# Performance work log

Hardware: AMD Instinct MI355X
Metric: run time of the kernel (lower is better)

## Reference

```python
import jax, jax.numpy as jnp
import numpy as np

# pywt db4 decomposition filters (w.dec_lo / w.dec_hi), full precision
DEC_LO = np.array([-0.010597401784997278, 0.032883011666982945, 0.030841381835986965,
                   -0.18703481171888114, -0.02798376941698385, 0.6308807679295904,
                   0.7148465705525415, 0.23037781330885523], dtype=np.float32)
DEC_HI = np.array([-0.23037781330885523, 0.7148465705525415, -0.6308807679295904,
                   -0.02798376941698385, 0.18703481171888114, 0.030841381835986965,
                   -0.032883011666982945, -0.010597401784997278], dtype=np.float32)
FLEN = 8
LEVELS = 4
# kernel for lax correlation == pywt convolution => use reversed dec filters
_KERN = np.stack([DEC_LO[::-1], DEC_HI[::-1]])[:, None, :]  # [2, 1, F]


def _dwt_step(x):
    """Single-level DWT matching pywt.dwt(x, 'db4', mode='symmetric').
    x: [N, L] -> (cA, cD) each [N, (L+F-1)//2].
    pywt: symmetric-extend by F-1 per side, full convolution with dec filter,
    keep conv[F-1:-(F-1)][1::2]  ==  correlation(ext[:,1:], reversed_filter, stride 2).
    """
    ext = jnp.pad(x, ((0, 0), (FLEN - 1, FLEN - 1)), mode='symmetric')[:, 1:]
    out = jax.lax.conv_general_dilated(
        ext[:, None, :],                      # [N, 1, Lext-1]
        jnp.asarray(_KERN, dtype=x.dtype),    # [2, 1, F]
        window_strides=(2,), padding='VALID') # [N, 2, o]
    return out[:, 0, :], out[:, 1, :]


def _features(c):
    """6 statistical features per signal. c: [N, L] -> [N, 6]."""
    absc = jnp.abs(c)
    sq = c * c
    mean_abs = absc.mean(-1)
    std = jnp.std(c, axis=-1)               # population std, matches np.std
    rms = jnp.sqrt(sq.mean(-1))
    mx = absc.max(-1)
    energy = sq.sum(-1)
    zc = (jnp.diff(jnp.sign(c), axis=-1) != 0).sum(-1).astype(c.dtype) / c.shape[-1]
    return jnp.stack([mean_abs, std, rms, mx, energy, zc], axis=-1)


def _wavelet_features(x2d):
    """x2d: [N, T] -> [N, 6*(LEVELS+1)] in pywt.wavedec coeff order."""
    cA = x2d
    cds = []
    for _ in range(LEVELS):
        cA, cD = _dwt_step(cA)
        cds.append(cD)
    coeffs = [cA] + cds[::-1]  # [cA4, cD4, cD3, cD2, cD1]
    return jnp.concatenate([_features(c) for c in coeffs], axis=-1)


def setup_inputs() -> dict:
    key = jax.random.key(0)
    x = jax.random.normal(key, (64, 64, 16384), dtype=jnp.float32)
    return {"x": x}


def reference(x):
    B, C, T = x.shape
    feats = _wavelet_features(x.reshape(B * C, T))  # [B*C, 30]
    return feats.reshape(B, C, -1)                  # [B, C, 30]
```

## Files before the change

kernel.cpp:

```cpp
#include <hip/hip_runtime.h>


#define T0 16384
#define BLK 512
#define NW (BLK / 64)

constexpr float FLO[8] = {
     0.23037781330885523f,  0.7148465705525415f,   0.6308807679295904f,
    -0.02798376941698385f, -0.18703481171888114f,  0.030841381835986965f,
     0.032883011666982945f, -0.010597401784997278f };
constexpr float FHI[8] = {
    -0.010597401784997278f, -0.032883011666982945f, 0.030841381835986965f,
     0.18703481171888114f,  -0.02798376941698385f,  -0.6308807679295904f,
     0.7148465705525415f,   -0.23037781330885523f };

__device__ __forceinline__ float getsym(const float* __restrict__ s, int t, int L) {
    if (t < 0) t = -1 - t;
    else if (t >= L) t = 2 * L - 1 - t;
    return s[t];
}

__device__ __forceinline__ float zcstep(float p, float q) {
    return ((__float_as_int(p) ^ __float_as_int(q)) < 0) ? 1.f : 0.f;
}

__device__ __forceinline__ void band_reduce(float sabs, float ssum, float ssq,
                                            float smax, float zc,
                                            int band, float* __restrict__ red) {
    #pragma unroll
    for (int off = 32; off > 0; off >>= 1) {
        sabs += __shfl_xor(sabs, off, 64);
        ssum += __shfl_xor(ssum, off, 64);
        ssq  += __shfl_xor(ssq,  off, 64);
        smax  = fmaxf(smax, __shfl_xor(smax, off, 64));
        zc   += __shfl_xor(zc,   off, 64);
    }
    const int lane = threadIdx.x & 63;
    const int wave = threadIdx.x >> 6;
    if (lane == 0) {
        float* r = red + (band * NW + wave) * 5;
        r[0] = sabs; r[1] = ssum; r[2] = ssq; r[3] = smax; r[4] = zc;
    }
}

template<bool LAST>
__device__ __forceinline__ void dwt_quad_level(const float* __restrict__ src, int L,
                                               float* __restrict__ dst, int o,
                                               int dband, float* __restrict__ red) {
    float sabs = 0.f, ssum = 0.f, ssq = 0.f, smax = 0.f, zc = 0.f;
    float sabsA = 0.f, ssumA = 0.f, ssqA = 0.f, smaxA = 0.f, zcA = 0.f;
    const int nq_main = (o - 1) >> 2;

    for (int k = threadIdx.x; k < nq_main; k += BLK) {
        const int w = 8 * k - 8;
        float v[20];
        if (w >= 0 && w + 20 <= L) {
            #pragma unroll
            for (int q = 0; q < 5; ++q) {
                const float4 t = *reinterpret_cast<const float4*>(src + w + 4 * q);
                v[4*q+0] = t.x; v[4*q+1] = t.y; v[4*q+2] = t.z; v[4*q+3] = t.w;
            }
        } else {
            #pragma unroll
            for (int j = 2; j < 18; ++j) v[j] = getsym(src, w + j, L);
        }
        float a[5], d[5];
        #pragma unroll
        for (int i = 0; i < 5; ++i) { a[i] = 0.f; d[i] = 0.f; }
        #pragma unroll
        for (int i = 0; i < 4; ++i) {
            #pragma unroll
            for (int m = 0; m < 8; ++m) {
                a[i] = fmaf(v[2*i+2+m], FLO[m], a[i]);
                d[i] = fmaf(v[2*i+2+m], FHI[m], d[i]);
            }
        }
        #pragma unroll
        for (int m = 0; m < 8; ++m) {
            d[4] = fmaf(v[10+m], FHI[m], d[4]);
            if constexpr (LAST) a[4] = fmaf(v[10+m], FLO[m], a[4]);
        }
        if constexpr (!LAST) {
            *reinterpret_cast<float4*>(dst + 4 * k) = make_float4(a[0], a[1], a[2], a[3]);
        }
        #pragma unroll
        for (int i = 0; i < 4; ++i) {
            const float ad = fabsf(d[i]);
            sabs += ad; ssum += d[i]; ssq = fmaf(d[i], d[i], ssq);
            smax = fmaxf(smax, ad);
            zc += zcstep(d[i], d[i+1]);
            if constexpr (LAST) {
                const float aa = fabsf(a[i]);
                sabsA += aa; ssumA += a[i]; ssqA = fmaf(a[i], a[i], ssqA);
                smaxA = fmaxf(smaxA, aa);
                zcA += zcstep(a[i], a[i+1]);
            }
        }
    }

    if (threadIdx.x == BLK - 1) {
        const int k = nq_main;
        const int w = 8 * k - 8;
        float v[20];
        #pragma unroll
        for (int j = 2; j < 18; ++j) v[j] = getsym(src, w + j, L);
        float a[5], d[5];
        #pragma unroll
        for (int i = 0; i < 5; ++i) { a[i] = 0.f; d[i] = 0.f; }
        #pragma unroll
        for (int i = 0; i < 5; ++i) {
            #pragma unroll
            for (int m = 0; m < 8; ++m) {
                a[i] = fmaf(v[2*i+2+m], FLO[m], a[i]);
                d[i] = fmaf(v[2*i+2+m], FHI[m], d[i]);
            }
        }
        #pragma unroll
        for (int i = 0; i < 4; ++i) {
            const int p = 4 * k + i;
            if (p < o) {
                const float ad = fabsf(d[i]);
                sabs += ad; ssum += d[i]; ssq = fmaf(d[i], d[i], ssq);
                smax = fmaxf(smax, ad);
                if (p + 1 < o) zc += zcstep(d[i], d[i+1]);
                if constexpr (LAST) {
                    const float aa = fabsf(a[i]);
                    sabsA += aa; ssumA += a[i]; ssqA = fmaf(a[i], a[i], ssqA);
                    smaxA = fmaxf(smaxA, aa);
                    if (p + 1 < o) zcA += zcstep(a[i], a[i+1]);
                } else {
                    dst[p] = a[i];
                }
            }
        }
    }

    band_reduce(sabs, ssum, ssq, smax, zc, dband, red);
    if constexpr (LAST) band_reduce(sabsA, ssumA, ssqA, smaxA, zcA, 0, red);
}

__global__ void __launch_bounds__(BLK, 6)
wavelet_feat_kernel(const float* __restrict__ x, float* __restrict__ out) {
    __shared__ __align__(16) float A[8196];
    __shared__ __align__(16) float B[4104];
    __shared__ float red[5 * NW * 5];

    const int sig = blockIdx.x;
    const float* src0 = x + (size_t)sig * T0;
    float* outp = out + (size_t)sig * 30;

    dwt_quad_level<false>(src0, T0,   A, 8195, 4, red);
    __syncthreads();
    dwt_quad_level<false>(A,    8195, B, 4101, 3, red);
    __syncthreads();
    dwt_quad_level<false>(B,    4101, A, 2054, 2, red);
    __syncthreads();
    dwt_quad_level<true >(A,    2054, nullptr, 1030, 1, red);
    __syncthreads();

    if (threadIdx.x < 5) {
        const int band = threadIdx.x;
        float a = 0.f, s = 0.f, q = 0.f, m = 0.f, z = 0.f;
        #pragma unroll
        for (int w = 0; w < NW; ++w) {
            const float* r = red + (band * NW + w) * 5;
            a += r[0]; s += r[1]; q += r[2]; m = fmaxf(m, r[3]); z += r[4];
        }
        const int o = (band <= 1) ? 1030 : (band == 2 ? 2054 : (band == 3 ? 4101 : 8195));
        const float inv  = 1.0f / (float)o;
        const float mean = s * inv;
        const float var  = q * inv - mean * mean;
        float* op = outp + band * 6;
        op[0] = a * inv;
        op[1] = sqrtf(fmaxf(var, 0.f));
        op[2] = sqrtf(q * inv);
        op[3] = m;
        op[4] = q;
        op[5] = z * inv;
    }
}

extern "C" void kernel_launch(void* const* d_in, const int* in_sizes, int n_in,
                              void* d_out, int out_size, void* d_ws, size_t ws_size,
                              hipStream_t stream) {
    const float* x = (const float*)d_in[0];
    float* out = (float*)d_out;
    const int nsig = in_sizes[0] / T0;
    hipLaunchKernelGGL(wavelet_feat_kernel, dim3(nsig), dim3(BLK), 0, stream, x, out);
}
```

Baseline: 90.06 us.

## Run DWT levels in place in one LDS buffer and reduce via ds_swizzle

```diff
diff --git a/kernel.cpp b/kernel.cpp
--- a/kernel.cpp
+++ b/kernel.cpp
@@ -3,7 +3,6 @@
 
 #define T0 16384
 #define BLK 512
-#define NW (BLK / 64)
 
 constexpr float FLO[8] = {
      0.23037781330885523f,  0.7148465705525415f,   0.6308807679295904f,
@@ -27,143 +26,196 @@
 __device__ __forceinline__ void band_reduce(float sabs, float ssum, float ssq,
                                             float smax, float zc,
                                             int band, float* __restrict__ red) {
-    #pragma unroll
-    for (int off = 32; off > 0; off >>= 1) {
-        sabs += __shfl_xor(sabs, off, 64);
-        ssum += __shfl_xor(ssum, off, 64);
-        ssq  += __shfl_xor(ssq,  off, 64);
-        smax  = fmaxf(smax, __shfl_xor(smax, off, 64));
-        zc   += __shfl_xor(zc,   off, 64);
-    }
-    const int lane = threadIdx.x & 63;
-    const int wave = threadIdx.x >> 6;
-    if (lane == 0) {
-        float* r = red + (band * NW + wave) * 5;
+#define SWZF(v, PAT) __int_as_float(__builtin_amdgcn_ds_swizzle(__float_as_int(v), PAT))
+#define RSTEP(PAT) \
+    sabs += SWZF(sabs, PAT); \
+    ssum += SWZF(ssum, PAT); \
+    ssq  += SWZF(ssq,  PAT); \
+    smax  = fmaxf(smax, SWZF(smax, PAT)); \
+    zc   += SWZF(zc,   PAT);
+    RSTEP(0x041F) RSTEP(0x081F) RSTEP(0x101F) RSTEP(0x201F) RSTEP(0x401F)
+#undef RSTEP
+#undef SWZF
+    if ((threadIdx.x & 31) == 0) {
+        float* r = red + (band * 16 + ((int)threadIdx.x >> 5)) * 5;
         r[0] = sabs; r[1] = ssum; r[2] = ssq; r[3] = smax; r[4] = zc;
     }
 }
 
+__device__ __forceinline__ void load_win(const float* __restrict__ src, int L, int k,
+                                         float* __restrict__ v) {
+    const int w = 8 * k - 8;
+    if (w >= 0 && w + 20 <= L) {
+        #pragma unroll
+        for (int q = 0; q < 5; ++q) {
+            const float4 t = *reinterpret_cast<const float4*>(src + w + 4 * q);
+            v[4*q+0] = t.x; v[4*q+1] = t.y; v[4*q+2] = t.z; v[4*q+3] = t.w;
+        }
+    } else {
+        #pragma unroll
+        for (int j = 2; j < 18; ++j) v[j] = getsym(src, w + j, L);
+    }
+}
+
 template<bool LAST>
-__device__ __forceinline__ void dwt_quad_level(const float* __restrict__ src, int L,
-                                               float* __restrict__ dst, int o,
-                                               int dband, float* __restrict__ red) {
+__device__ __forceinline__ void quad_dots(const float* __restrict__ v,
+                                          float* __restrict__ a, float* __restrict__ d) {
+    #pragma unroll
+    for (int i = 0; i < 5; ++i) { a[i] = 0.f; d[i] = 0.f; }
+    #pragma unroll
+    for (int i = 0; i < 4; ++i) {
+        #pragma unroll
+        for (int m = 0; m < 8; ++m) {
+            a[i] = fmaf(v[2*i+2+m], FLO[m], a[i]);
+            d[i] = fmaf(v[2*i+2+m], FHI[m], d[i]);
+        }
+    }
+    #pragma unroll
+    for (int m = 0; m < 8; ++m) {
+        d[4] = fmaf(v[10+m], FHI[m], d[4]);
+        if constexpr (LAST) a[4] = fmaf(v[10+m], FLO[m], a[4]);
+    }
+}
+
+__device__ void dwt_l1(const float* __restrict__ x, float* __restrict__ A,
+                       float* __restrict__ red) {
     float sabs = 0.f, ssum = 0.f, ssq = 0.f, smax = 0.f, zc = 0.f;
-    float sabsA = 0.f, ssumA = 0.f, ssqA = 0.f, smaxA = 0.f, zcA = 0.f;
-    const int nq_main = (o - 1) >> 2;
-
-    for (int k = threadIdx.x; k < nq_main; k += BLK) {
-        const int w = 8 * k - 8;
-        float v[20];
-        if (w >= 0 && w + 20 <= L) {
-            #pragma unroll
-            for (int q = 0; q < 5; ++q) {
-                const float4 t = *reinterpret_cast<const float4*>(src + w + 4 * q);
-                v[4*q+0] = t.x; v[4*q+1] = t.y; v[4*q+2] = t.z; v[4*q+3] = t.w;
-            }
-        } else {
-            #pragma unroll
-            for (int j = 2; j < 18; ++j) v[j] = getsym(src, w + j, L);
-        }
-        float a[5], d[5];
-        #pragma unroll
-        for (int i = 0; i < 5; ++i) { a[i] = 0.f; d[i] = 0.f; }
-        #pragma unroll
-        for (int i = 0; i < 4; ++i) {
-            #pragma unroll
-            for (int m = 0; m < 8; ++m) {
-                a[i] = fmaf(v[2*i+2+m], FLO[m], a[i]);
-                d[i] = fmaf(v[2*i+2+m], FHI[m], d[i]);
-            }
-        }
-        #pragma unroll
-        for (int m = 0; m < 8; ++m) {
-            d[4] = fmaf(v[10+m], FHI[m], d[4]);
-            if constexpr (LAST) a[4] = fmaf(v[10+m], FLO[m], a[4]);
-        }
-        if constexpr (!LAST) {
-            *reinterpret_cast<float4*>(dst + 4 * k) = make_float4(a[0], a[1], a[2], a[3]);
-        }
+    const int L = T0;
+    for (int k = (int)threadIdx.x; k < 2048; k += BLK) {
+        float v[20], a[5], d[5];
+        load_win(x, L, k, v);
+        quad_dots<false>(v, a, d);
+        *reinterpret_cast<float4*>(A + 4 * k) = make_float4(a[0], a[1], a[2], a[3]);
         #pragma unroll
         for (int i = 0; i < 4; ++i) {
             const float ad = fabsf(d[i]);
             sabs += ad; ssum += d[i]; ssq = fmaf(d[i], d[i], ssq);
             smax = fmaxf(smax, ad);
-            zc += zcstep(d[i], d[i+1]);
-            if constexpr (LAST) {
-                const float aa = fabsf(a[i]);
-                sabsA += aa; ssumA += a[i]; ssqA = fmaf(a[i], a[i], ssqA);
-                smaxA = fmaxf(smaxA, aa);
-                zcA += zcstep(a[i], a[i+1]);
-            }
-        }
-    }
-
+            zc += zcstep(d[i], d[i + 1]);
+        }
+    }
     if (threadIdx.x == BLK - 1) {
-        const int k = nq_main;
-        const int w = 8 * k - 8;
-        float v[20];
-        #pragma unroll
-        for (int j = 2; j < 18; ++j) v[j] = getsym(src, w + j, L);
-        float a[5], d[5];
-        #pragma unroll
-        for (int i = 0; i < 5; ++i) { a[i] = 0.f; d[i] = 0.f; }
-        #pragma unroll
-        for (int i = 0; i < 5; ++i) {
-            #pragma unroll
-            for (int m = 0; m < 8; ++m) {
-                a[i] = fmaf(v[2*i+2+m], FLO[m], a[i]);
-                d[i] = fmaf(v[2*i+2+m], FHI[m], d[i]);
-            }
-        }
+        const int k = 2048;
+        float v[20], a[5], d[5];
+        #pragma unroll
+        for (int j = 2; j < 18; ++j) v[j] = getsym(x, 8 * k - 8 + j, L);
+        quad_dots<false>(v, a, d);
+        #pragma unroll
+        for (int m = 0; m < 8; ++m) a[4] = fmaf(v[10 + m], FLO[m], a[4]);
         #pragma unroll
         for (int i = 0; i < 4; ++i) {
             const int p = 4 * k + i;
-            if (p < o) {
+            if (p < 8195) {
+                A[p] = a[i];
                 const float ad = fabsf(d[i]);
                 sabs += ad; ssum += d[i]; ssq = fmaf(d[i], d[i], ssq);
                 smax = fmaxf(smax, ad);
-                if (p + 1 < o) zc += zcstep(d[i], d[i+1]);
+                if (p + 1 < 8195) zc += zcstep(d[i], d[i + 1]);
+            }
+        }
+    }
+    band_reduce(sabs, ssum, ssq, smax, zc, 4, red);
+}
+
+template<bool LAST, int L, int o, int DBAND>
+__device__ __forceinline__ void dwt_ip(float* __restrict__ A, float* __restrict__ red) {
+    float sabs = 0.f, ssum = 0.f, ssq = 0.f, smax = 0.f, zc = 0.f;
+    float sabsA = 0.f, ssumA = 0.f, ssqA = 0.f, smaxA = 0.f, zcA = 0.f;
+    constexpr int NQ  = (o - 1) >> 2;
+    constexpr int NCH = (NQ + BLK - 1) / BLK;
+    const int tid = (int)threadIdx.x;
+
+    float ap[4];  int wk = -1;
+    float tq[4];  bool tw = false;
+
+    #pragma unroll
+    for (int c = 0; c < NCH; ++c) {
+        const int k = c * BLK + tid;
+        wk = -1;
+        if (k < NQ) {
+            float v[20], a[5], d[5];
+            load_win(A, L, k, v);
+            quad_dots<LAST>(v, a, d);
+            #pragma unroll
+            for (int i = 0; i < 4; ++i) {
+                const float ad = fabsf(d[i]);
+                sabs += ad; ssum += d[i]; ssq = fmaf(d[i], d[i], ssq);
+                smax = fmaxf(smax, ad);
+                zc += zcstep(d[i], d[i + 1]);
                 if constexpr (LAST) {
                     const float aa = fabsf(a[i]);
                     sabsA += aa; ssumA += a[i]; ssqA = fmaf(a[i], a[i], ssqA);
                     smaxA = fmaxf(smaxA, aa);
-                    if (p + 1 < o) zcA += zcstep(a[i], a[i+1]);
-                } else {
-                    dst[p] = a[i];
+                    zcA += zcstep(a[i], a[i + 1]);
                 }
             }
-        }
-    }
-
-    band_reduce(sabs, ssum, ssq, smax, zc, dband, red);
+            ap[0] = a[0]; ap[1] = a[1]; ap[2] = a[2]; ap[3] = a[3];
+            wk = k;
+        }
+        if (c == NCH - 1 && tid == BLK - 1) {
+            float v[20], a[5], d[5];
+            #pragma unroll
+            for (int j = 2; j < 18; ++j) v[j] = getsym(A, 8 * NQ - 8 + j, L);
+            quad_dots<true>(v, a, d);
+            #pragma unroll
+            for (int i = 0; i < 4; ++i) {
+                const int p = 4 * NQ + i;
+                if (p < o) {
+                    const float ad = fabsf(d[i]);
+                    sabs += ad; ssum += d[i]; ssq = fmaf(d[i], d[i], ssq);
+                    smax = fmaxf(smax, ad);
+                    if (p + 1 < o) zc += zcstep(d[i], d[i + 1]);
+                    if constexpr (LAST) {
+                        const float aa = fabsf(a[i]);
+                        sabsA += aa; ssumA += a[i]; ssqA = fmaf(a[i], a[i], ssqA);
+                        smaxA = fmaxf(smaxA, aa);
+                        if (p + 1 < o) zcA += zcstep(a[i], a[i + 1]);
+                    }
+                }
+                tq[i] = a[i];
+            }
+            tw = true;
+        }
+        if constexpr (!LAST) {
+            __syncthreads();
+            if (wk >= 0)
+                *reinterpret_cast<float4*>(A + 4 * wk) = make_float4(ap[0], ap[1], ap[2], ap[3]);
+            if (tw) {
+                #pragma unroll
+                for (int i = 0; i < 4; ++i)
+                    if (4 * NQ + i < o) A[4 * NQ + i] = tq[i];
+                tw = false;
+            }
+        }
+    }
+    band_reduce(sabs, ssum, ssq, smax, zc, DBAND, red);
     if constexpr (LAST) band_reduce(sabsA, ssumA, ssqA, smaxA, zcA, 0, red);
 }
 
-__global__ void __launch_bounds__(BLK, 6)
+__global__ void __launch_bounds__(BLK, 8)
 wavelet_feat_kernel(const float* __restrict__ x, float* __restrict__ out) {
     __shared__ __align__(16) float A[8196];
-    __shared__ __align__(16) float B[4104];
-    __shared__ float red[5 * NW * 5];
+    __shared__ float red[5 * 16 * 5];
 
     const int sig = blockIdx.x;
     const float* src0 = x + (size_t)sig * T0;
     float* outp = out + (size_t)sig * 30;
 
-    dwt_quad_level<false>(src0, T0,   A, 8195, 4, red);
-    __syncthreads();
-    dwt_quad_level<false>(A,    8195, B, 4101, 3, red);
-    __syncthreads();
-    dwt_quad_level<false>(B,    4101, A, 2054, 2, red);
-    __syncthreads();
-    dwt_quad_level<true >(A,    2054, nullptr, 1030, 1, red);
+    dwt_l1(src0, A, red);
+    __syncthreads();
+    dwt_ip<false, 8195, 4101, 3>(A, red);
+    __syncthreads();
+    dwt_ip<false, 4101, 2054, 2>(A, red);
+    __syncthreads();
+    dwt_ip<true,  2054, 1030, 1>(A, red);
     __syncthreads();
 
     if (threadIdx.x < 5) {
-        const int band = threadIdx.x;
+        const int band = (int)threadIdx.x;
         float a = 0.f, s = 0.f, q = 0.f, m = 0.f, z = 0.f;
         #pragma unroll
-        for (int w = 0; w < NW; ++w) {
-            const float* r = red + (band * NW + w) * 5;
+        for (int h = 0; h < 16; ++h) {
+            const float* r = red + (band * 16 + h) * 5;
             a += r[0]; s += r[1]; q += r[2]; m = fmaxf(m, r[3]); z += r[4];
         }
         const int o = (band <= 1) ? 1030 : (band == 2 ? 2054 : (band == 3 ? 4101 : 8195));
```

Measured after the change: 103.6 us. 1.15x slower.

## Compute DWT levels in place in registers to drop second LDS buffer

Applied to the files above, without the earlier changes.

```diff
diff --git a/kernel.cpp b/kernel.cpp
--- a/kernel.cpp
+++ b/kernel.cpp
@@ -43,6 +43,55 @@
     }
 }
 
+__device__ __forceinline__ void load_win(const float* __restrict__ src, int L, int k,
+                                         float* __restrict__ v) {
+    const int w = 8 * k - 8;
+    if (w >= 0 && w + 20 <= L) {
+        #pragma unroll
+        for (int q = 0; q < 5; ++q) {
+            const float4 t = *reinterpret_cast<const float4*>(src + w + 4 * q);
+            v[4*q+0] = t.x; v[4*q+1] = t.y; v[4*q+2] = t.z; v[4*q+3] = t.w;
+        }
+    } else {
+        #pragma unroll
+        for (int j = 2; j < 18; ++j) v[j] = getsym(src, w + j, L);
+    }
+}
+
+template<bool LAST>
+__device__ __forceinline__ void quad_dots(const float* __restrict__ v,
+                                          float* __restrict__ a, float* __restrict__ d) {
+    #pragma unroll
+    for (int i = 0; i < 5; ++i) { a[i] = 0.f; d[i] = 0.f; }
+    #pragma unroll
+    for (int i = 0; i < 4; ++i) {
+        #pragma unroll
+        for (int m = 0; m < 8; ++m) {
+            a[i] = fmaf(v[2*i+2+m], FLO[m], a[i]);
+            d[i] = fmaf(v[2*i+2+m], FHI[m], d[i]);
+        }
+    }
+    #pragma unroll
+    for (int m = 0; m < 8; ++m) {
+        d[4] = fmaf(v[10+m], FHI[m], d[4]);
+        if constexpr (LAST) a[4] = fmaf(v[10+m], FLO[m], a[4]);
+    }
+}
+
+__device__ __forceinline__ void quad_dots_tail(const float* __restrict__ v,
+                                               float* __restrict__ a, float* __restrict__ d) {
+    #pragma unroll
+    for (int i = 0; i < 5; ++i) { a[i] = 0.f; d[i] = 0.f; }
+    #pragma unroll
+    for (int i = 0; i < 5; ++i) {
+        #pragma unroll
+        for (int m = 0; m < 8; ++m) {
+            a[i] = fmaf(v[2*i+2+m], FLO[m], a[i]);
+            d[i] = fmaf(v[2*i+2+m], FHI[m], d[i]);
+        }
+    }
+}
+
 template<bool LAST>
 __device__ __forceinline__ void dwt_quad_level(const float* __restrict__ src, int L,
                                                float* __restrict__ dst, int o,
@@ -52,34 +101,9 @@
     const int nq_main = (o - 1) >> 2;
 
     for (int k = threadIdx.x; k < nq_main; k += BLK) {
-        const int w = 8 * k - 8;
-        float v[20];
-        if (w >= 0 && w + 20 <= L) {
-            #pragma unroll
-            for (int q = 0; q < 5; ++q) {
-                const float4 t = *reinterpret_cast<const float4*>(src + w + 4 * q);
-                v[4*q+0] = t.x; v[4*q+1] = t.y; v[4*q+2] = t.z; v[4*q+3] = t.w;
-            }
-        } else {
-            #pragma unroll
-            for (int j = 2; j < 18; ++j) v[j] = getsym(src, w + j, L);
-        }
-        float a[5], d[5];
-        #pragma unroll
-        for (int i = 0; i < 5; ++i) { a[i] = 0.f; d[i] = 0.f; }
-        #pragma unroll
-        for (int i = 0; i < 4; ++i) {
-            #pragma unroll
-            for (int m = 0; m < 8; ++m) {
-                a[i] = fmaf(v[2*i+2+m], FLO[m], a[i]);
-                d[i] = fmaf(v[2*i+2+m], FHI[m], d[i]);
-            }
-        }
-        #pragma unroll
-        for (int m = 0; m < 8; ++m) {
-            d[4] = fmaf(v[10+m], FHI[m], d[4]);
-            if constexpr (LAST) a[4] = fmaf(v[10+m], FLO[m], a[4]);
-        }
+        float v[20], a[5], d[5];
+        load_win(src, L, k, v);
+        quad_dots<LAST>(v, a, d);
         if constexpr (!LAST) {
             *reinterpret_cast<float4*>(dst + 4 * k) = make_float4(a[0], a[1], a[2], a[3]);
         }
@@ -88,33 +112,22 @@
             const float ad = fabsf(d[i]);
             sabs += ad; ssum += d[i]; ssq = fmaf(d[i], d[i], ssq);
             smax = fmaxf(smax, ad);
-            zc += zcstep(d[i], d[i+1]);
+            zc += zcstep(d[i], d[i + 1]);
             if constexpr (LAST) {
                 const float aa = fabsf(a[i]);
                 sabsA += aa; ssumA += a[i]; ssqA = fmaf(a[i], a[i], ssqA);
                 smaxA = fmaxf(smaxA, aa);
-                zcA += zcstep(a[i], a[i+1]);
+                zcA += zcstep(a[i], a[i + 1]);
             }
         }
     }
 
     if (threadIdx.x == BLK - 1) {
         const int k = nq_main;
-        const int w = 8 * k - 8;
-        float v[20];
-        #pragma unroll
-        for (int j = 2; j < 18; ++j) v[j] = getsym(src, w + j, L);
-        float a[5], d[5];
-        #pragma unroll
-        for (int i = 0; i < 5; ++i) { a[i] = 0.f; d[i] = 0.f; }
-        #pragma unroll
-        for (int i = 0; i < 5; ++i) {
-            #pragma unroll
-            for (int m = 0; m < 8; ++m) {
-                a[i] = fmaf(v[2*i+2+m], FLO[m], a[i]);
-                d[i] = fmaf(v[2*i+2+m], FHI[m], d[i]);
-            }
-        }
+        float v[20], a[5], d[5];
+        #pragma unroll
+        for (int j = 2; j < 18; ++j) v[j] = getsym(src, 8 * k - 8 + j, L);
+        quad_dots_tail(v, a, d);
         #pragma unroll
         for (int i = 0; i < 4; ++i) {
             const int p = 4 * k + i;
@@ -139,27 +152,88 @@
     if constexpr (LAST) band_reduce(sabsA, ssumA, ssqA, smaxA, zcA, 0, red);
 }
 
-__global__ void __launch_bounds__(BLK, 6)
+template<int L, int o, int DBAND>
+__device__ __forceinline__ void dwt_hold_level(float* __restrict__ A,
+                                               float* __restrict__ red) {
+    float sabs = 0.f, ssum = 0.f, ssq = 0.f, smax = 0.f, zc = 0.f;
+    constexpr int NQ = (o - 1) >> 2;
+    constexpr int NI = (NQ + BLK - 1) / BLK;
+    const int tid = (int)threadIdx.x;
+
+    float hq[NI][4];
+    float tq[4];
+
+    #pragma unroll
+    for (int c = 0; c < NI; ++c) {
+        const int k = c * BLK + tid;
+        if (k < NQ) {
+            float v[20], a[5], d[5];
+            load_win(A, L, k, v);
+            quad_dots<false>(v, a, d);
+            #pragma unroll
+            for (int i = 0; i < 4; ++i) {
+                const float ad = fabsf(d[i]);
+                sabs += ad; ssum += d[i]; ssq = fmaf(d[i], d[i], ssq);
+                smax = fmaxf(smax, ad);
+                zc += zcstep(d[i], d[i + 1]);
+                hq[c][i] = a[i];
+            }
+        }
+    }
+    if (tid == BLK - 1) {
+        float v[20], a[5], d[5];
+        #pragma unroll
+        for (int j = 2; j < 18; ++j) v[j] = getsym(A, 8 * NQ - 8 + j, L);
+        quad_dots_tail(v, a, d);
+        #pragma unroll
+        for (int i = 0; i < 4; ++i) {
+            const int p = 4 * NQ + i;
+            if (p < o) {
+                const float ad = fabsf(d[i]);
+                sabs += ad; ssum += d[i]; ssq = fmaf(d[i], d[i], ssq);
+                smax = fmaxf(smax, ad);
+                if (p + 1 < o) zc += zcstep(d[i], d[i + 1]);
+            }
+            tq[i] = a[i];
+        }
+    }
+
+    __syncthreads();
+    #pragma unroll
+    for (int c = 0; c < NI; ++c) {
+        const int k = c * BLK + tid;
+        if (k < NQ)
+            *reinterpret_cast<float4*>(A + 4 * k) =
+                make_float4(hq[c][0], hq[c][1], hq[c][2], hq[c][3]);
+    }
+    if (tid == BLK - 1) {
+        #pragma unroll
+        for (int i = 0; i < 4; ++i)
+            if (4 * NQ + i < o) A[4 * NQ + i] = tq[i];
+    }
+    __syncthreads();
+
+    band_reduce(sabs, ssum, ssq, smax, zc, DBAND, red);
+}
+
+__global__ void __launch_bounds__(BLK, 8)
 wavelet_feat_kernel(const float* __restrict__ x, float* __restrict__ out) {
     __shared__ __align__(16) float A[8196];
-    __shared__ __align__(16) float B[4104];
     __shared__ float red[5 * NW * 5];
 
     const int sig = blockIdx.x;
     const float* src0 = x + (size_t)sig * T0;
     float* outp = out + (size_t)sig * 30;
 
-    dwt_quad_level<false>(src0, T0,   A, 8195, 4, red);
-    __syncthreads();
-    dwt_quad_level<false>(A,    8195, B, 4101, 3, red);
-    __syncthreads();
-    dwt_quad_level<false>(B,    4101, A, 2054, 2, red);
-    __syncthreads();
-    dwt_quad_level<true >(A,    2054, nullptr, 1030, 1, red);
+    dwt_quad_level<false>(src0, T0, A, 8195, 4, red);
+    __syncthreads();
+    dwt_hold_level<8195, 4101, 3>(A, red);
+    dwt_hold_level<4101, 2054, 2>(A, red);
+    dwt_quad_level<true>(A, 2054, nullptr, 1030, 1, red);
     __syncthreads();
 
     if (threadIdx.x < 5) {
-        const int band = threadIdx.x;
+        const int band = (int)threadIdx.x;
         float a = 0.f, s = 0.f, q = 0.f, m = 0.f, z = 0.f;
         #pragma unroll
         for (int w = 0; w < NW; ++w) {
```

Result: slower. 131.3 us (+45.8%).

## Give each thread a contiguous span per level with swizzled LDS and bitmask zero-crossings

Applied to the files above, without the earlier changes.

```diff
diff --git a/kernel.cpp b/kernel.cpp
--- a/kernel.cpp
+++ b/kernel.cpp
@@ -14,152 +14,167 @@
      0.18703481171888114f,  -0.02798376941698385f,  -0.6308807679295904f,
      0.7148465705525415f,   -0.23037781330885523f };
 
-__device__ __forceinline__ float getsym(const float* __restrict__ s, int t, int L) {
-    if (t < 0) t = -1 - t;
-    else if (t >= L) t = 2 * L - 1 - t;
-    return s[t];
-}
-
-__device__ __forceinline__ float zcstep(float p, float q) {
-    return ((__float_as_int(p) ^ __float_as_int(q)) < 0) ? 1.f : 0.f;
-}
-
-__device__ __forceinline__ void band_reduce(float sabs, float ssum, float ssq,
-                                            float smax, float zc,
-                                            int band, float* __restrict__ red) {
+#define SWZ(i4) ((i4) ^ (((i4) >> 3) & 7))
+
+__device__ __forceinline__ float4 lds_read4(const float* __restrict__ A, int i4) {
+    return reinterpret_cast<const float4*>(A)[SWZ(i4)];
+}
+__device__ __forceinline__ void lds_write4(float* __restrict__ A, int i4, float4 t) {
+    reinterpret_cast<float4*>(A)[SWZ(i4)] = t;
+}
+__device__ __forceinline__ void lds_write1(float* __restrict__ A, int f, float t) {
+    A[4 * SWZ(f >> 2) + (f & 3)] = t;
+}
+
+struct Acc { float sabs, ssum, ssq, smax, zc; };
+
+__device__ __forceinline__ void band_reduce(Acc a, int band, float* __restrict__ red) {
     #pragma unroll
     for (int off = 32; off > 0; off >>= 1) {
-        sabs += __shfl_xor(sabs, off, 64);
-        ssum += __shfl_xor(ssum, off, 64);
-        ssq  += __shfl_xor(ssq,  off, 64);
-        smax  = fmaxf(smax, __shfl_xor(smax, off, 64));
-        zc   += __shfl_xor(zc,   off, 64);
+        a.sabs += __shfl_xor(a.sabs, off, 64);
+        a.ssum += __shfl_xor(a.ssum, off, 64);
+        a.ssq  += __shfl_xor(a.ssq,  off, 64);
+        a.smax  = fmaxf(a.smax, __shfl_xor(a.smax, off, 64));
+        a.zc   += __shfl_xor(a.zc,   off, 64);
     }
     const int lane = threadIdx.x & 63;
     const int wave = threadIdx.x >> 6;
     if (lane == 0) {
         float* r = red + (band * NW + wave) * 5;
-        r[0] = sabs; r[1] = ssum; r[2] = ssq; r[3] = smax; r[4] = zc;
-    }
-}
-
-template<bool LAST>
-__device__ __forceinline__ void dwt_quad_level(const float* __restrict__ src, int L,
-                                               float* __restrict__ dst, int o,
-                                               int dband, float* __restrict__ red) {
-    float sabs = 0.f, ssum = 0.f, ssq = 0.f, smax = 0.f, zc = 0.f;
-    float sabsA = 0.f, ssumA = 0.f, ssqA = 0.f, smaxA = 0.f, zcA = 0.f;
-    const int nq_main = (o - 1) >> 2;
-
-    for (int k = threadIdx.x; k < nq_main; k += BLK) {
-        const int w = 8 * k - 8;
-        float v[20];
-        if (w >= 0 && w + 20 <= L) {
-            #pragma unroll
-            for (int q = 0; q < 5; ++q) {
-                const float4 t = *reinterpret_cast<const float4*>(src + w + 4 * q);
-                v[4*q+0] = t.x; v[4*q+1] = t.y; v[4*q+2] = t.z; v[4*q+3] = t.w;
+        r[0] = a.sabs; r[1] = a.ssum; r[2] = a.ssq; r[3] = a.smax; r[4] = a.zc;
+    }
+}
+
+template<int NOUT, bool EXTRA, bool LAST, bool VECW>
+__device__ __forceinline__ void span_core(const float* __restrict__ v,
+                                          float* __restrict__ dst, int p0,
+                                          Acc& aD, Acc& aA) {
+    unsigned dm = 0, am = 0;
+    float aq[4];
+    #pragma unroll
+    for (int i = 0; i < NOUT; ++i) {
+        float a = 0.f, d = 0.f;
+        #pragma unroll
+        for (int m = 0; m < 8; ++m) {
+            a = fmaf(v[2*i+2+m], FLO[m], a);
+            d = fmaf(v[2*i+2+m], FHI[m], d);
+        }
+        dm = (dm << 1) | (__float_as_uint(d) >> 31);
+        aD.sabs += fabsf(d); aD.ssum += d; aD.ssq = fmaf(d, d, aD.ssq);
+        aD.smax = fmaxf(aD.smax, fabsf(d));
+        if constexpr (LAST) {
+            am = (am << 1) | (__float_as_uint(a) >> 31);
+            aA.sabs += fabsf(a); aA.ssum += a; aA.ssq = fmaf(a, a, aA.ssq);
+            aA.smax = fmaxf(aA.smax, fabsf(a));
+        } else if constexpr (VECW) {
+            aq[i & 3] = a;
+            if ((i & 3) == 3)
+                lds_write4(dst, (p0 >> 2) + (i >> 2),
+                           make_float4(aq[0], aq[1], aq[2], aq[3]));
+        } else {
+            lds_write1(dst, p0 + i, a);
+        }
+    }
+    if constexpr (EXTRA) {
+        float d = 0.f;
+        #pragma unroll
+        for (int m = 0; m < 8; ++m) d = fmaf(v[2*NOUT+2+m], FHI[m], d);
+        dm = (dm << 1) | (__float_as_uint(d) >> 31);
+        if constexpr (LAST) {
+            float a = 0.f;
+            #pragma unroll
+            for (int m = 0; m < 8; ++m) a = fmaf(v[2*NOUT+2+m], FLO[m], a);
+            am = (am << 1) | (__float_as_uint(a) >> 31);
+        }
+    }
+    constexpr int NP = EXTRA ? NOUT : NOUT - 1;
+    if constexpr (NP > 0) {
+        aD.zc += (float)__popc((dm ^ (dm >> 1)) & ((1u << NP) - 1u));
+        if constexpr (LAST)
+            aA.zc += (float)__popc((am ^ (am >> 1)) & ((1u << NP) - 1u));
+    }
+}
+
+template<int S, int NT, int L, int o, bool LAST, bool GSRC>
+__device__ __forceinline__ void dwt_level(const float* __restrict__ src,
+                                          float* __restrict__ dst,
+                                          int dband, float* __restrict__ red) {
+    Acc aD = {0.f, 0.f, 0.f, 0.f, 0.f};
+    Acc aA = {0.f, 0.f, 0.f, 0.f, 0.f};
+    const int t = (int)threadIdx.x;
+    constexpr int SN = o - S * (NT - 1);
+
+    if (t < NT - 1) {
+        constexpr int NF = S / 2 + 3;
+        float v[4 * NF];
+        const int w = 2 * S * t - 8;
+        if (t == 0) {
+            #pragma unroll
+            for (int q = 0; q < NF - 2; ++q) {
+                float4 f;
+                if constexpr (GSRC) f = *reinterpret_cast<const float4*>(src + 4 * q);
+                else                f = lds_read4(src, q);
+                v[8+4*q] = f.x; v[9+4*q] = f.y; v[10+4*q] = f.z; v[11+4*q] = f.w;
             }
+            #pragma unroll
+            for (int j = 0; j < 8; ++j) v[j] = v[15 - j];
         } else {
             #pragma unroll
-            for (int j = 2; j < 18; ++j) v[j] = getsym(src, w + j, L);
-        }
-        float a[5], d[5];
-        #pragma unroll
-        for (int i = 0; i < 5; ++i) { a[i] = 0.f; d[i] = 0.f; }
-        #pragma unroll
-        for (int i = 0; i < 4; ++i) {
-            #pragma unroll
-            for (int m = 0; m < 8; ++m) {
-                a[i] = fmaf(v[2*i+2+m], FLO[m], a[i]);
-                d[i] = fmaf(v[2*i+2+m], FHI[m], d[i]);
+            for (int q = 0; q < NF; ++q) {
+                float4 f;
+                if constexpr (GSRC) f = *reinterpret_cast<const float4*>(src + w + 4 * q);
+                else                f = lds_read4(src, (w >> 2) + q);
+                v[4*q] = f.x; v[4*q+1] = f.y; v[4*q+2] = f.z; v[4*q+3] = f.w;
             }
         }
-        #pragma unroll
-        for (int m = 0; m < 8; ++m) {
-            d[4] = fmaf(v[10+m], FHI[m], d[4]);
-            if constexpr (LAST) a[4] = fmaf(v[10+m], FLO[m], a[4]);
-        }
-        if constexpr (!LAST) {
-            *reinterpret_cast<float4*>(dst + 4 * k) = make_float4(a[0], a[1], a[2], a[3]);
-        }
-        #pragma unroll
-        for (int i = 0; i < 4; ++i) {
-            const float ad = fabsf(d[i]);
-            sabs += ad; ssum += d[i]; ssq = fmaf(d[i], d[i], ssq);
-            smax = fmaxf(smax, ad);
-            zc += zcstep(d[i], d[i+1]);
-            if constexpr (LAST) {
-                const float aa = fabsf(a[i]);
-                sabsA += aa; ssumA += a[i]; ssqA = fmaf(a[i], a[i], ssqA);
-                smaxA = fmaxf(smaxA, aa);
-                zcA += zcstep(a[i], a[i+1]);
+        span_core<S, true, LAST, true>(v, dst, S * t, aD, aA);
+    } else if (t == NT - 1) {
+        constexpr int NFt = (2 * SN + 8 + 3) / 4;
+        constexpr int p0 = S * (NT - 1);
+        constexpr int w  = 2 * p0 - 8;
+        constexpr int JM = L - w;
+        float v[4 * NFt];
+        #pragma unroll
+        for (int q = 0; q < NFt; ++q) {
+            if (!GSRC || (w + 4 * q + 4 <= L)) {
+                float4 f;
+                if constexpr (GSRC) f = *reinterpret_cast<const float4*>(src + w + 4 * q);
+                else                f = lds_read4(src, (w >> 2) + q);
+                v[4*q] = f.x; v[4*q+1] = f.y; v[4*q+2] = f.z; v[4*q+3] = f.w;
             }
         }
-    }
-
-    if (threadIdx.x == BLK - 1) {
-        const int k = nq_main;
-        const int w = 8 * k - 8;
-        float v[20];
-        #pragma unroll
-        for (int j = 2; j < 18; ++j) v[j] = getsym(src, w + j, L);
-        float a[5], d[5];
-        #pragma unroll
-        for (int i = 0; i < 5; ++i) { a[i] = 0.f; d[i] = 0.f; }
-        #pragma unroll
-        for (int i = 0; i < 5; ++i) {
-            #pragma unroll
-            for (int m = 0; m < 8; ++m) {
-                a[i] = fmaf(v[2*i+2+m], FLO[m], a[i]);
-                d[i] = fmaf(v[2*i+2+m], FHI[m], d[i]);
-            }
-        }
-        #pragma unroll
-        for (int i = 0; i < 4; ++i) {
-            const int p = 4 * k + i;
-            if (p < o) {
-                const float ad = fabsf(d[i]);
-                sabs += ad; ssum += d[i]; ssq = fmaf(d[i], d[i], ssq);
-                smax = fmaxf(smax, ad);
-                if (p + 1 < o) zc += zcstep(d[i], d[i+1]);
-                if constexpr (LAST) {
-                    const float aa = fabsf(a[i]);
-                    sabsA += aa; ssumA += a[i]; ssqA = fmaf(a[i], a[i], ssqA);
-                    smaxA = fmaxf(smaxA, aa);
-                    if (p + 1 < o) zcA += zcstep(a[i], a[i+1]);
-                } else {
-                    dst[p] = a[i];
-                }
-            }
-        }
-    }
-
-    band_reduce(sabs, ssum, ssq, smax, zc, dband, red);
-    if constexpr (LAST) band_reduce(sabsA, ssumA, ssqA, smaxA, zcA, 0, red);
+        #pragma unroll
+        for (int j = JM; j < 4 * NFt; ++j)
+            v[j] = v[2 * JM - 1 - j];
+        span_core<SN, false, LAST, false>(v, dst, p0, aD, aA);
+    }
+
+    band_reduce(aD, dband, red);
+    if constexpr (LAST) band_reduce(aA, 0, red);
 }
 
 __global__ void __launch_bounds__(BLK, 6)
 wavelet_feat_kernel(const float* __restrict__ x, float* __restrict__ out) {
-    __shared__ __align__(16) float A[8196];
-    __shared__ __align__(16) float B[4104];
+    __shared__ float4 A4[2056];
+    __shared__ float4 B4[1032];
     __shared__ float red[5 * NW * 5];
-
-    const int sig = blockIdx.x;
-    const float* src0 = x + (size_t)sig * T0;
-    float* outp = out + (size_t)sig * 30;
-
-    dwt_quad_level<false>(src0, T0,   A, 8195, 4, red);
-    __syncthreads();
-    dwt_quad_level<false>(A,    8195, B, 4101, 3, red);
-    __syncthreads();
-    dwt_quad_level<false>(B,    4101, A, 2054, 2, red);
-    __syncthreads();
-    dwt_quad_level<true >(A,    2054, nullptr, 1030, 1, red);
+    float* A = reinterpret_cast<float*>(A4);
+    float* B = reinterpret_cast<float*>(B4);
+
+    const float* src0 = x + (size_t)blockIdx.x * T0;
+    float* outp = out + (size_t)blockIdx.x * 30;
+
+    dwt_level<16, 512, 16384, 8195, false, true >(src0, A, 4, red);
+    __syncthreads();
+    dwt_level< 8, 512,  8195, 4101, false, false>(A,    B, 3, red);
+    __syncthreads();
+    dwt_level< 4, 512,  4101, 2054, false, false>(B,    A, 2, red);
+    __syncthreads();
+    dwt_level< 4, 257,  2054, 1030, true,  false>(A, nullptr, 1, red);
     __syncthreads();
 
     if (threadIdx.x < 5) {
-        const int band = threadIdx.x;
+        const int band = (int)threadIdx.x;
         float a = 0.f, s = 0.f, q = 0.f, m = 0.f, z = 0.f;
         #pragma unroll
         for (int w = 0; w < NW; ++w) {
```

New measurement: 91.81 us. Within noise of the previous version (+1.9%).
